# Performance work log

Measured on AMD Instinct MI355X. Metric: run time of the kernel, lower is better.

## Reference

```python
import jax, jax.numpy as jnp
import numpy as np

NEG = -9e15

def setup_inputs() -> dict:
    key = jax.random.key(0)
    k_h, k_adj, k_W, k_bW, k_a1, k_b1, k_a2, k_b2 = jax.random.split(key, 8)
    N, IN, OUT = 8192, 512, 512
    h = jax.random.normal(k_h, (N, IN), dtype=jnp.float32)
    adj = jax.random.randint(k_adj, (N, N), 0, 2, dtype=jnp.int32)
    # torch Linear default init: U(-1/sqrt(fan_in), 1/sqrt(fan_in))
    s_in = 1.0 / np.sqrt(IN)
    s_out = 1.0 / np.sqrt(OUT)
    W = jax.random.uniform(k_W, (IN, OUT), minval=-s_in, maxval=s_in, dtype=jnp.float32)
    bW = jax.random.uniform(k_bW, (OUT,), minval=-s_in, maxval=s_in, dtype=jnp.float32)
    a1 = jax.random.uniform(k_a1, (OUT,), minval=-s_out, maxval=s_out, dtype=jnp.float32)
    b1 = jax.random.uniform(k_b1, (), minval=-s_out, maxval=s_out, dtype=jnp.float32)
    a2 = jax.random.uniform(k_a2, (OUT,), minval=-s_out, maxval=s_out, dtype=jnp.float32)
    b2 = jax.random.uniform(k_b2, (), minval=-s_out, maxval=s_out, dtype=jnp.float32)
    return {"h": h, "adj": adj, "W": W, "bW": bW, "a1": a1, "b1": b1, "a2": a2, "b2": b2}

def reference(h, adj, W, bW, a1, b1, a2, b2):
    alpha = 0.2
    # Wh: [N, OUT]; dropout is identity at inference (training=False)
    Wh = h @ W + bW
    Wha1 = Wh @ a1 + b1  # [N]
    Wha2 = Wh @ a2 + b2  # [N]
    e = Wha1[:, None] + Wha2[None, :]  # [N, N] broadcast additive scores
    e = jnp.where(e > 0, e, alpha * e)  # leaky relu
    e = jnp.where(adj > 0, e, jnp.float32(-9e15))
    attention = jax.nn.softmax(e, axis=1)
    h_prime = attention @ Wh  # [N, OUT]
    return h_prime
```

## Files before the change

kernel.cpp:

```cpp
#include <hip/hip_runtime.h>
#include <stdint.h>


#define NN 8192
#define DD 512

typedef __attribute__((ext_vector_type(8))) short short8;
typedef __attribute__((ext_vector_type(4))) float f32x4;
typedef __attribute__((ext_vector_type(4))) float float4v;
typedef __attribute__((ext_vector_type(4))) unsigned short ushort4v;

__device__ __forceinline__ uint16_t f2bf(float f) {
  union { float f; uint32_t u; } v; v.f = f;
  uint32_t u = v.u;
  u += 0x7fffu + ((u >> 16) & 1u);
  return (uint16_t)(u >> 16);
}
__device__ __forceinline__ float bf2f(uint16_t b) {
  union { uint32_t u; float f; } v; v.u = ((uint32_t)b) << 16;
  return v.f;
}

__device__ __forceinline__ void async_copy16(uint16_t* lds, const uint16_t* g) {
  __builtin_amdgcn_global_load_lds(
      (const __attribute__((address_space(1))) uint32_t*)g,
      (__attribute__((address_space(3))) uint32_t*)lds, 16, 0, 0);
}

__global__ __launch_bounds__(256) void conv_wt(const float* __restrict__ W,
                                               uint16_t* __restrict__ WT) {
  __shared__ float ts[64][65];
  int tid = threadIdx.x;
  int kt = (blockIdx.x >> 3) * 64, ct = (blockIdx.x & 7) * 64;
  #pragma unroll
  for (int it = 0; it < 4; ++it) {
    int idx = it * 256 + tid;
    int r = idx >> 4, q = idx & 15;
    float4v v = *(const float4v*)(W + (size_t)(kt + r) * 512 + ct + q * 4);
    ts[r][q * 4 + 0] = v.x; ts[r][q * 4 + 1] = v.y;
    ts[r][q * 4 + 2] = v.z; ts[r][q * 4 + 3] = v.w;
  }
  __syncthreads();
  #pragma unroll
  for (int it = 0; it < 4; ++it) {
    int idx = it * 256 + tid;
    int c = idx >> 4, q = idx & 15;
    ushort4v p;
    p.x = f2bf(ts[q * 4 + 0][c]); p.y = f2bf(ts[q * 4 + 1][c]);
    p.z = f2bf(ts[q * 4 + 2][c]); p.w = f2bf(ts[q * 4 + 3][c]);
    *(ushort4v*)(WT + (size_t)(ct + c) * 512 + kt + q * 4) = p;
  }
}

__global__ __launch_bounds__(512) void wh_gemm(const float* __restrict__ h,
                                               const uint16_t* __restrict__ WT,
                                               const float* __restrict__ bW,
                                               const float* __restrict__ a1,
                                               const float* __restrict__ a2,
                                               uint16_t* __restrict__ WhT,
                                               float* __restrict__ s1g,
                                               float* __restrict__ s2g) {
  __shared__ __align__(16) uint16_t At[32 * 32];
  __shared__ __align__(16) uint16_t Bt[512 * 32];
  __shared__ float s1loc[32], s2loc[32];
  int tid = threadIdx.x;
  int wave = tid >> 6, lane = tid & 63;
  int l15 = lane & 15, quad = lane >> 4;
  int i0 = blockIdx.x * 32;
  if (tid < 32) { s1loc[tid] = 0.f; s2loc[tid] = 0.f; }
  f32x4 acc[2][4] = {};
  for (int k0 = 0; k0 < 512; k0 += 32) {
    if (tid < 256) {
      int r = tid >> 3, ks = (tid & 7) * 4;
      float4v hv = *(const float4v*)(h + (size_t)(i0 + r) * 512 + k0 + ks);
      ushort4v p;
      p.x = f2bf(hv.x); p.y = f2bf(hv.y); p.z = f2bf(hv.z); p.w = f2bf(hv.w);
      *(ushort4v*)&At[r * 32 + ks] = p;
    }
    #pragma unroll
    for (int rr = 0; rr < 4; ++rr) {
      int idx = rr * 512 + tid;
      int c = idx >> 2, q = idx & 3;
      async_copy16(&Bt[idx * 8], WT + c * 512 + k0 + q * 8);
    }
    __syncthreads();
    short8 a0 = *(const short8*)&At[l15 * 32 + quad * 8];
    short8 a1f = *(const short8*)&At[(l15 + 16) * 32 + quad * 8];
    #pragma unroll
    for (int nt = 0; nt < 4; ++nt) {
      int c = wave * 64 + nt * 16 + l15;
      short8 b = *(const short8*)&Bt[c * 32 + quad * 8];
      acc[0][nt] = __builtin_amdgcn_mfma_f32_16x16x32_bf16(a0, b, acc[0][nt], 0, 0, 0);
      acc[1][nt] = __builtin_amdgcn_mfma_f32_16x16x32_bf16(a1f, b, acc[1][nt], 0, 0, 0);
    }
    __syncthreads();
  }
  #pragma unroll
  for (int mt = 0; mt < 2; ++mt) {
    int ib = i0 + mt * 16 + quad * 4;
    float r1[4] = {0.f, 0.f, 0.f, 0.f};
    float r2[4] = {0.f, 0.f, 0.f, 0.f};
    #pragma unroll
    for (int nt = 0; nt < 4; ++nt) {
      int c = wave * 64 + nt * 16 + l15;
      float bias = bW[c];
      float a1c = a1[c], a2c = a2[c];
      float v0 = acc[mt][nt].x + bias;
      float v1 = acc[mt][nt].y + bias;
      float v2 = acc[mt][nt].z + bias;
      float v3 = acc[mt][nt].w + bias;
      ushort4v p;
      p.x = f2bf(v0); p.y = f2bf(v1); p.z = f2bf(v2); p.w = f2bf(v3);
      *(ushort4v*)&WhT[(size_t)c * 8192 + ib] = p;
      r1[0] = fmaf(v0, a1c, r1[0]); r1[1] = fmaf(v1, a1c, r1[1]);
      r1[2] = fmaf(v2, a1c, r1[2]); r1[3] = fmaf(v3, a1c, r1[3]);
      r2[0] = fmaf(v0, a2c, r2[0]); r2[1] = fmaf(v1, a2c, r2[1]);
      r2[2] = fmaf(v2, a2c, r2[2]); r2[3] = fmaf(v3, a2c, r2[3]);
    }
    #pragma unroll
    for (int v = 0; v < 4; ++v) {
      int row = mt * 16 + quad * 4 + v;
      atomicAdd(&s1loc[row], r1[v]);
      atomicAdd(&s2loc[row], r2[v]);
    }
  }
  __syncthreads();
  if (tid < 32) {
    s1g[i0 + tid] = s1loc[tid];
    s2g[i0 + tid] = s2loc[tid];
  }
}

__global__ __launch_bounds__(256) void w_k(const int* __restrict__ adj,
                                           const float* __restrict__ s1,
                                           const float* __restrict__ s2,
                                           const float* __restrict__ b1,
                                           const float* __restrict__ b2,
                                           uint16_t* __restrict__ w,
                                           float* __restrict__ dinv) {
  __shared__ float wsum[4];
  int i = blockIdx.x;
  int tid = threadIdx.x;
  float base = s1[i] + b1[0] + b2[0];
  const int* arow = adj + (size_t)i * 8192;
  uint16_t* wrow = w + (size_t)i * 8192;
  float sum = 0.f;
  #pragma unroll
  for (int it = 0; it < 8; ++it) {
    int j = it * 1024 + tid * 4;
    int4 av = *(const int4*)(arow + j);
    float4v sv = *(const float4v*)(s2 + j);
    float e, wv;
    ushort4v p;
    e = base + sv.x; e = fmaxf(e, 0.2f * e);
    wv = (av.x > 0) ? __expf(e) : 0.f; p.x = f2bf(wv); sum += bf2f(p.x);
    e = base + sv.y; e = fmaxf(e, 0.2f * e);
    wv = (av.y > 0) ? __expf(e) : 0.f; p.y = f2bf(wv); sum += bf2f(p.y);
    e = base + sv.z; e = fmaxf(e, 0.2f * e);
    wv = (av.z > 0) ? __expf(e) : 0.f; p.z = f2bf(wv); sum += bf2f(p.z);
    e = base + sv.w; e = fmaxf(e, 0.2f * e);
    wv = (av.w > 0) ? __expf(e) : 0.f; p.w = f2bf(wv); sum += bf2f(p.w);
    *(ushort4v*)(wrow + j) = p;
  }
  #pragma unroll
  for (int o = 32; o > 0; o >>= 1) sum += __shfl_down(sum, o);
  if ((tid & 63) == 0) wsum[tid >> 6] = sum;
  __syncthreads();
  if (tid == 0) dinv[i] = 1.0f / (wsum[0] + wsum[1] + wsum[2] + wsum[3]);
}

__global__ __launch_bounds__(512, 8) void pv_gemm(const uint16_t* __restrict__ w,
                                                  const uint16_t* __restrict__ WhT,
                                                  const float* __restrict__ dinv,
                                                  float* __restrict__ out) {
  __shared__ __align__(16) uint16_t At[32 * 128];
  __shared__ __align__(16) uint16_t Bt[128 * 128];
  int tid = threadIdx.x;
  int wave = tid >> 6, lane = tid & 63;
  int l15 = lane & 15, quad = lane >> 4;
  int rb = blockIdx.x & 255, cb = blockIdx.x >> 8;
  int i0 = rb * 32, c0 = cb * 128;
  f32x4 acc[2] = {};
  int ar = tid >> 4, ap = tid & 15;
  int asc = ap ^ (ar & 15);
  const uint16_t* aptr = w + (size_t)(i0 + ar) * 8192 + asc * 8;
  for (int j0 = 0; j0 < 8192; j0 += 128) {
    async_copy16(&At[tid * 8], aptr + j0);
    #pragma unroll
    for (int it = 0; it < 4; ++it) {
      int idx = it * 512 + tid;
      int r = idx >> 4, p = idx & 15;
      int sc = p ^ (r & 15);
      async_copy16(&Bt[idx * 8], WhT + (size_t)(c0 + r) * 8192 + j0 + sc * 8);
    }
    __syncthreads();
    int brow = wave * 16 + l15;
    #pragma unroll
    for (int ks = 0; ks < 4; ++ks) {
      int ch = ks * 4 + quad;
      short8 b = *(const short8*)&Bt[brow * 128 + ((ch ^ (brow & 15)) * 8)];
      #pragma unroll
      for (int rt = 0; rt < 2; ++rt) {
        int arow = rt * 16 + l15;
        short8 a = *(const short8*)&At[arow * 128 + ((ch ^ (arow & 15)) * 8)];
        acc[rt] = __builtin_amdgcn_mfma_f32_16x16x32_bf16(a, b, acc[rt], 0, 0, 0);
      }
    }
    __syncthreads();
  }
  #pragma unroll
  for (int rt = 0; rt < 2; ++rt) {
    #pragma unroll
    for (int v = 0; v < 4; ++v) {
      int rloc = rt * 16 + quad * 4 + v;
      float dv = dinv[i0 + rloc];
      out[(size_t)(i0 + rloc) * 512 + c0 + wave * 16 + l15] = acc[rt][v] * dv;
    }
  }
}

__global__ __launch_bounds__(512) void attn_k(const int* __restrict__ adj,
                                              const float* __restrict__ s1,
                                              const float* __restrict__ s2,
                                              const float* __restrict__ b1,
                                              const float* __restrict__ b2,
                                              const uint16_t* __restrict__ WhT,
                                              float* __restrict__ out) {
  __shared__ __align__(16) uint16_t At[32 * 32];
  __shared__ __align__(16) uint16_t Bt[512 * 32];
  __shared__ float dred[512];
  __shared__ float dinv[32];
  int tid = threadIdx.x;
  int wave = tid >> 6, lane = tid & 63;
  int l15 = lane & 15, quad = lane >> 4;
  int i0 = blockIdx.x * 32;
  int wr = tid >> 4;
  int wc = (tid & 15) * 2;
  float s1v = s1[i0 + wr] + b1[0] + b2[0];
  float dpart = 0.f;
  f32x4 acc[2][4] = {};
  const int* adjrow = adj + (size_t)(i0 + wr) * 8192 + wc;
  for (int j0 = 0; j0 < 8192; j0 += 32) {
    int2 av = *(const int2*)(adjrow + j0);
    float2 s2v = *(const float2*)(s2 + j0 + wc);
    float e0 = s1v + s2v.x; e0 = fmaxf(e0, 0.2f * e0);
    float e1 = s1v + s2v.y; e1 = fmaxf(e1, 0.2f * e1);
    float w0 = (av.x > 0) ? __expf(e0) : 0.f;
    float w1 = (av.y > 0) ? __expf(e1) : 0.f;
    dpart += w0 + w1;
    uint32_t packed = (uint32_t)f2bf(w0) | ((uint32_t)f2bf(w1) << 16);
    *(uint32_t*)&At[wr * 32 + wc] = packed;
    #pragma unroll
    for (int rr = 0; rr < 4; ++rr) {
      int idx = rr * 512 + tid;
      int c = idx >> 2, q = idx & 3;
      async_copy16(&Bt[idx * 8], WhT + (size_t)c * 8192 + j0 + q * 8);
    }
    __syncthreads();
    short8 a0 = *(const short8*)&At[l15 * 32 + quad * 8];
    short8 a1f = *(const short8*)&At[(l15 + 16) * 32 + quad * 8];
    #pragma unroll
    for (int nt = 0; nt < 4; ++nt) {
      short8 b = *(const short8*)&Bt[(wave * 64 + nt * 16 + l15) * 32 + quad * 8];
      acc[0][nt] = __builtin_amdgcn_mfma_f32_16x16x32_bf16(a0, b, acc[0][nt], 0, 0, 0);
      acc[1][nt] = __builtin_amdgcn_mfma_f32_16x16x32_bf16(a1f, b, acc[1][nt], 0, 0, 0);
    }
    __syncthreads();
  }
  dred[tid] = dpart;
  __syncthreads();
  if (tid < 32) {
    float s = 0.f;
    #pragma unroll
    for (int q = 0; q < 16; ++q) s += dred[tid * 16 + q];
    dinv[tid] = 1.0f / s;
  }
  __syncthreads();
  #pragma unroll
  for (int mt = 0; mt < 2; ++mt) {
    #pragma unroll
    for (int nt = 0; nt < 4; ++nt) {
      int c = wave * 64 + nt * 16 + l15;
      #pragma unroll
      for (int v = 0; v < 4; ++v) {
        int row = mt * 16 + quad * 4 + v;
        out[(size_t)(i0 + row) * 512 + c] = acc[mt][nt][v] * dinv[row];
      }
    }
  }
}

extern "C" void kernel_launch(void* const* d_in, const int* in_sizes, int n_in,
                              void* d_out, int out_size, void* d_ws, size_t ws_size,
                              hipStream_t stream) {
  const float* h   = (const float*)d_in[0];
  const int*   adj = (const int*)d_in[1];
  const float* W   = (const float*)d_in[2];
  const float* bW  = (const float*)d_in[3];
  const float* a1  = (const float*)d_in[4];
  const float* b1  = (const float*)d_in[5];
  const float* a2  = (const float*)d_in[6];
  const float* b2  = (const float*)d_in[7];
  float* out = (float*)d_out;
  char* ws = (char*)d_ws;

  const size_t NEED = 143228928ULL;
  if (ws_size >= NEED) {
    uint16_t* w   = (uint16_t*)(ws);
    uint16_t* WhT = (uint16_t*)(ws + 134217728);
    uint16_t* WT  = (uint16_t*)(ws + 142606336);
    float* s1     = (float*)(ws + 143130624);
    float* s2     = (float*)(ws + 143163392);
    float* dinv   = (float*)(ws + 143196160);

    conv_wt<<<64, 256, 0, stream>>>(W, WT);
    wh_gemm<<<256, 512, 0, stream>>>(h, WT, bW, a1, a2, WhT, s1, s2);
    w_k<<<8192, 256, 0, stream>>>(adj, s1, s2, b1, b2, w, dinv);
    pv_gemm<<<1024, 512, 0, stream>>>(w, WhT, dinv, out);
  } else {
    uint16_t* WhT = (uint16_t*)(ws);
    uint16_t* WT  = (uint16_t*)(ws + 8388608);
    float* s1     = (float*)(ws + 8912896);
    float* s2     = (float*)(ws + 8945664);

    conv_wt<<<64, 256, 0, stream>>>(W, WT);
    wh_gemm<<<256, 512, 0, stream>>>(h, WT, bW, a1, a2, WhT, s1, s2);
    attn_k<<<256, 512, 0, stream>>>(adj, s1, s2, b1, b2, WhT, out);
  }
}
```

Before: 584.6 us.

## Fuse attention weight generation into the PV GEMM, removing the bf16 weight matrix

Replaces the two-kernel path (materialise an 8192x8192 bf16 weight matrix, then GEMM it with Wh) with one fused kernel. The new kernel computes masked exp weights from adj on the fly into a swizzled LDS tile and multiplies them against a 256-column slice of WhT. Each 32-row block is split across two column halves, so the adjacency and exp work is done twice. Adjacency loads are prefetched one tile ahead and block indices are remapped so that paired column blocks share rows. This removes the 128MB write and read of the intermediate matrix, at the cost of duplicated elementwise work and a larger LDS footprint.

```diff
diff --git a/kernel.cpp b/kernel.cpp
--- a/kernel.cpp
+++ b/kernel.cpp
@@ -131,139 +131,81 @@
   }
 }
 
-__global__ __launch_bounds__(256) void w_k(const int* __restrict__ adj,
-                                           const float* __restrict__ s1,
-                                           const float* __restrict__ s2,
-                                           const float* __restrict__ b1,
-                                           const float* __restrict__ b2,
-                                           uint16_t* __restrict__ w,
-                                           float* __restrict__ dinv) {
-  __shared__ float wsum[4];
-  int i = blockIdx.x;
-  int tid = threadIdx.x;
-  float base = s1[i] + b1[0] + b2[0];
-  const int* arow = adj + (size_t)i * 8192;
-  uint16_t* wrow = w + (size_t)i * 8192;
-  float sum = 0.f;
-  #pragma unroll
-  for (int it = 0; it < 8; ++it) {
-    int j = it * 1024 + tid * 4;
-    int4 av = *(const int4*)(arow + j);
-    float4v sv = *(const float4v*)(s2 + j);
-    float e, wv;
-    ushort4v p;
-    e = base + sv.x; e = fmaxf(e, 0.2f * e);
-    wv = (av.x > 0) ? __expf(e) : 0.f; p.x = f2bf(wv); sum += bf2f(p.x);
-    e = base + sv.y; e = fmaxf(e, 0.2f * e);
-    wv = (av.y > 0) ? __expf(e) : 0.f; p.y = f2bf(wv); sum += bf2f(p.y);
-    e = base + sv.z; e = fmaxf(e, 0.2f * e);
-    wv = (av.z > 0) ? __expf(e) : 0.f; p.z = f2bf(wv); sum += bf2f(p.z);
-    e = base + sv.w; e = fmaxf(e, 0.2f * e);
-    wv = (av.w > 0) ? __expf(e) : 0.f; p.w = f2bf(wv); sum += bf2f(p.w);
-    *(ushort4v*)(wrow + j) = p;
-  }
-  #pragma unroll
-  for (int o = 32; o > 0; o >>= 1) sum += __shfl_down(sum, o);
-  if ((tid & 63) == 0) wsum[tid >> 6] = sum;
-  __syncthreads();
-  if (tid == 0) dinv[i] = 1.0f / (wsum[0] + wsum[1] + wsum[2] + wsum[3]);
-}
-
-__global__ __launch_bounds__(512, 8) void pv_gemm(const uint16_t* __restrict__ w,
-                                                  const uint16_t* __restrict__ WhT,
-                                                  const float* __restrict__ dinv,
-                                                  float* __restrict__ out) {
+__global__ __launch_bounds__(512, 4) void attn2(const int* __restrict__ adj,
+                                                const float* __restrict__ s1,
+                                                const float* __restrict__ s2,
+                                                const float* __restrict__ b1,
+                                                const float* __restrict__ b2,
+                                                const uint16_t* __restrict__ WhT,
+                                                float* __restrict__ out) {
   __shared__ __align__(16) uint16_t At[32 * 128];
-  __shared__ __align__(16) uint16_t Bt[128 * 128];
+  __shared__ __align__(16) uint16_t Bt[256 * 128];
+  __shared__ float dred[512];
+  __shared__ float dloc[32];
   int tid = threadIdx.x;
   int wave = tid >> 6, lane = tid & 63;
   int l15 = lane & 15, quad = lane >> 4;
-  int rb = blockIdx.x & 255, cb = blockIdx.x >> 8;
-  int i0 = rb * 32, c0 = cb * 128;
-  f32x4 acc[2] = {};
-  int ar = tid >> 4, ap = tid & 15;
-  int asc = ap ^ (ar & 15);
-  const uint16_t* aptr = w + (size_t)(i0 + ar) * 8192 + asc * 8;
+  int x = blockIdx.x;
+  int cb = (x >> 3) & 1;
+  int rb = (x & 7) | ((x >> 4) << 3);
+  int i0 = rb * 32, c0 = cb * 256;
+  int wr = tid >> 4, p = tid & 15;
+  float s1v = s1[i0 + wr] + b1[0] + b2[0];
+  const int* adjp = adj + (size_t)(i0 + wr) * 8192 + p * 8;
+  const float* s2p = s2 + p * 8;
+  uint16_t* awp = &At[wr * 128 + ((p ^ (wr & 15)) * 8)];
+  float dpart = 0.f;
+  f32x4 acc[2][2] = {};
+  int4 av0 = *(const int4*)(adjp);
+  int4 av1 = *(const int4*)(adjp + 4);
   for (int j0 = 0; j0 < 8192; j0 += 128) {
-    async_copy16(&At[tid * 8], aptr + j0);
-    #pragma unroll
-    for (int it = 0; it < 4; ++it) {
+    #pragma unroll
+    for (int it = 0; it < 8; ++it) {
       int idx = it * 512 + tid;
-      int r = idx >> 4, p = idx & 15;
-      int sc = p ^ (r & 15);
+      int r = idx >> 4, pp = idx & 15;
+      int sc = pp ^ (r & 15);
       async_copy16(&Bt[idx * 8], WhT + (size_t)(c0 + r) * 8192 + j0 + sc * 8);
     }
-    __syncthreads();
-    int brow = wave * 16 + l15;
+    int jn = (j0 + 128) & 8191;
+    int4 nv0 = *(const int4*)(adjp + jn);
+    int4 nv1 = *(const int4*)(adjp + jn + 4);
+    float4v sv0 = *(const float4v*)(s2p + j0);
+    float4v sv1 = *(const float4v*)(s2p + j0 + 4);
+    short8 pk;
+    float e, wv;
+    uint16_t b;
+    e = s1v + sv0.x; e = fmaxf(e, 0.2f * e);
+    wv = (av0.x > 0) ? __expf(e) : 0.f; b = f2bf(wv); pk[0] = (short)b; dpart += bf2f(b);
+    e = s1v + sv0.y; e = fmaxf(e, 0.2f * e);
+    wv = (av0.y > 0) ? __expf(e) : 0.f; b = f2bf(wv); pk[1] = (short)b; dpart += bf2f(b);
+    e = s1v + sv0.z; e = fmaxf(e, 0.2f * e);
+    wv = (av0.z > 0) ? __expf(e) : 0.f; b = f2bf(wv); pk[2] = (short)b; dpart += bf2f(b);
+    e = s1v + sv0.w; e = fmaxf(e, 0.2f * e);
+    wv = (av0.w > 0) ? __expf(e) : 0.f; b = f2bf(wv); pk[3] = (short)b; dpart += bf2f(b);
+    e = s1v + sv1.x; e = fmaxf(e, 0.2f * e);
+    wv = (av1.x > 0) ? __expf(e) : 0.f; b = f2bf(wv); pk[4] = (short)b; dpart += bf2f(b);
+    e = s1v + sv1.y; e = fmaxf(e, 0.2f * e);
+    wv = (av1.y > 0) ? __expf(e) : 0.f; b = f2bf(wv); pk[5] = (short)b; dpart += bf2f(b);
+    e = s1v + sv1.z; e = fmaxf(e, 0.2f * e);
+    wv = (av1.z > 0) ? __expf(e) : 0.f; b = f2bf(wv); pk[6] = (short)b; dpart += bf2f(b);
+    e = s1v + sv1.w; e = fmaxf(e, 0.2f * e);
+    wv = (av1.w > 0) ? __expf(e) : 0.f; b = f2bf(wv); pk[7] = (short)b; dpart += bf2f(b);
+    *(short8*)awp = pk;
+    av0 = nv0; av1 = nv1;
+    __syncthreads();
+    int brow0 = wave * 32 + l15;
+    int brow1 = brow0 + 16;
     #pragma unroll
     for (int ks = 0; ks < 4; ++ks) {
       int ch = ks * 4 + quad;
-      short8 b = *(const short8*)&Bt[brow * 128 + ((ch ^ (brow & 15)) * 8)];
-      #pragma unroll
-      for (int rt = 0; rt < 2; ++rt) {
-        int arow = rt * 16 + l15;
-        short8 a = *(const short8*)&At[arow * 128 + ((ch ^ (arow & 15)) * 8)];
-        acc[rt] = __builtin_amdgcn_mfma_f32_16x16x32_bf16(a, b, acc[rt], 0, 0, 0);
-      }
-    }
-    __syncthreads();
-  }
-  #pragma unroll
-  for (int rt = 0; rt < 2; ++rt) {
-    #pragma unroll
-    for (int v = 0; v < 4; ++v) {
-      int rloc = rt * 16 + quad * 4 + v;
-      float dv = dinv[i0 + rloc];
-      out[(size_t)(i0 + rloc) * 512 + c0 + wave * 16 + l15] = acc[rt][v] * dv;
-    }
-  }
-}
-
-__global__ __launch_bounds__(512) void attn_k(const int* __restrict__ adj,
-                                              const float* __restrict__ s1,
-                                              const float* __restrict__ s2,
-                                              const float* __restrict__ b1,
-                                              const float* __restrict__ b2,
-                                              const uint16_t* __restrict__ WhT,
-                                              float* __restrict__ out) {
-  __shared__ __align__(16) uint16_t At[32 * 32];
-  __shared__ __align__(16) uint16_t Bt[512 * 32];
-  __shared__ float dred[512];
-  __shared__ float dinv[32];
-  int tid = threadIdx.x;
-  int wave = tid >> 6, lane = tid & 63;
-  int l15 = lane & 15, quad = lane >> 4;
-  int i0 = blockIdx.x * 32;
-  int wr = tid >> 4;
-  int wc = (tid & 15) * 2;
-  float s1v = s1[i0 + wr] + b1[0] + b2[0];
-  float dpart = 0.f;
-  f32x4 acc[2][4] = {};
-  const int* adjrow = adj + (size_t)(i0 + wr) * 8192 + wc;
-  for (int j0 = 0; j0 < 8192; j0 += 32) {
-    int2 av = *(const int2*)(adjrow + j0);
-    float2 s2v = *(const float2*)(s2 + j0 + wc);
-    float e0 = s1v + s2v.x; e0 = fmaxf(e0, 0.2f * e0);
-    float e1 = s1v + s2v.y; e1 = fmaxf(e1, 0.2f * e1);
-    float w0 = (av.x > 0) ? __expf(e0) : 0.f;
-    float w1 = (av.y > 0) ? __expf(e1) : 0.f;
-    dpart += w0 + w1;
-    uint32_t packed = (uint32_t)f2bf(w0) | ((uint32_t)f2bf(w1) << 16);
-    *(uint32_t*)&At[wr * 32 + wc] = packed;
-    #pragma unroll
-    for (int rr = 0; rr < 4; ++rr) {
-      int idx = rr * 512 + tid;
-      int c = idx >> 2, q = idx & 3;
-      async_copy16(&Bt[idx * 8], WhT + (size_t)c * 8192 + j0 + q * 8);
-    }
-    __syncthreads();
-    short8 a0 = *(const short8*)&At[l15 * 32 + quad * 8];
-    short8 a1f = *(const short8*)&At[(l15 + 16) * 32 + quad * 8];
-    #pragma unroll
-    for (int nt = 0; nt < 4; ++nt) {
-      short8 b = *(const short8*)&Bt[(wave * 64 + nt * 16 + l15) * 32 + quad * 8];
-      acc[0][nt] = __builtin_amdgcn_mfma_f32_16x16x32_bf16(a0, b, acc[0][nt], 0, 0, 0);
-      acc[1][nt] = __builtin_amdgcn_mfma_f32_16x16x32_bf16(a1f, b, acc[1][nt], 0, 0, 0);
+      short8 b0 = *(const short8*)&Bt[brow0 * 128 + ((ch ^ l15) * 8)];
+      short8 b1f = *(const short8*)&Bt[brow1 * 128 + ((ch ^ l15) * 8)];
+      short8 am0 = *(const short8*)&At[l15 * 128 + ((ch ^ l15) * 8)];
+      short8 am1 = *(const short8*)&At[(l15 + 16) * 128 + ((ch ^ l15) * 8)];
+      acc[0][0] = __builtin_amdgcn_mfma_f32_16x16x32_bf16(am0, b0, acc[0][0], 0, 0, 0);
+      acc[0][1] = __builtin_amdgcn_mfma_f32_16x16x32_bf16(am0, b1f, acc[0][1], 0, 0, 0);
+      acc[1][0] = __builtin_amdgcn_mfma_f32_16x16x32_bf16(am1, b0, acc[1][0], 0, 0, 0);
+      acc[1][1] = __builtin_amdgcn_mfma_f32_16x16x32_bf16(am1, b1f, acc[1][1], 0, 0, 0);
     }
     __syncthreads();
   }
@@ -273,18 +215,18 @@
     float s = 0.f;
     #pragma unroll
     for (int q = 0; q < 16; ++q) s += dred[tid * 16 + q];
-    dinv[tid] = 1.0f / s;
+    dloc[tid] = 1.0f / s;
   }
   __syncthreads();
   #pragma unroll
   for (int mt = 0; mt < 2; ++mt) {
     #pragma unroll
-    for (int nt = 0; nt < 4; ++nt) {
-      int c = wave * 64 + nt * 16 + l15;
+    for (int nt = 0; nt < 2; ++nt) {
+      int c = c0 + wave * 32 + nt * 16 + l15;
       #pragma unroll
       for (int v = 0; v < 4; ++v) {
         int row = mt * 16 + quad * 4 + v;
-        out[(size_t)(i0 + row) * 512 + c] = acc[mt][nt][v] * dinv[row];
+        out[(size_t)(i0 + row) * 512 + c] = acc[mt][nt][v] * dloc[row];
       }
     }
   }
@@ -304,27 +246,12 @@
   float* out = (float*)d_out;
   char* ws = (char*)d_ws;
 
-  const size_t NEED = 143228928ULL;
-  if (ws_size >= NEED) {
-    uint16_t* w   = (uint16_t*)(ws);
-    uint16_t* WhT = (uint16_t*)(ws + 134217728);
-    uint16_t* WT  = (uint16_t*)(ws + 142606336);
-    float* s1     = (float*)(ws + 143130624);
-    float* s2     = (float*)(ws + 143163392);
-    float* dinv   = (float*)(ws + 143196160);
-
-    conv_wt<<<64, 256, 0, stream>>>(W, WT);
-    wh_gemm<<<256, 512, 0, stream>>>(h, WT, bW, a1, a2, WhT, s1, s2);
-    w_k<<<8192, 256, 0, stream>>>(adj, s1, s2, b1, b2, w, dinv);
-    pv_gemm<<<1024, 512, 0, stream>>>(w, WhT, dinv, out);
-  } else {
-    uint16_t* WhT = (uint16_t*)(ws);
-    uint16_t* WT  = (uint16_t*)(ws + 8388608);
-    float* s1     = (float*)(ws + 8912896);
-    float* s2     = (float*)(ws + 8945664);
-
-    conv_wt<<<64, 256, 0, stream>>>(W, WT);
-    wh_gemm<<<256, 512, 0, stream>>>(h, WT, bW, a1, a2, WhT, s1, s2);
-    attn_k<<<256, 512, 0, stream>>>(adj, s1, s2, b1, b2, WhT, out);
-  }
-}
+  uint16_t* WhT = (uint16_t*)(ws);
+  uint16_t* WT  = (uint16_t*)(ws + 8388608);
+  float* s1     = (float*)(ws + 8912896);
+  float* s2     = (float*)(ws + 8945664);
+
+  conv_wt<<<64, 256, 0, stream>>>(W, WT);
+  wh_gemm<<<256, 512, 0, stream>>>(h, WT, bW, a1, a2, WhT, s1, s2);
+  attn2<<<512, 512, 0, stream>>>(adj, s1, s2, b1, b2, WhT, out);
+}
```

New measurement: 548.7 us. 6.1% less time.
